# Kernel tuning notes

Hardware: AMD Instinct MI355X
Metric: run time of the kernel (lower is better)

## Reference

```python
import jax, jax.numpy as jnp
import numpy as np
from jax import lax

B, F_BINS, T = 4, 196, 1000
DM, H, DEPTH, FFN, L, EDIM = 512, 8, 64, 2048, 4, 128


def setup_inputs() -> dict:
    key = jax.random.key(0)
    ks = jax.random.split(key, 16)
    d = {}
    d['spec'] = jax.random.normal(ks[0], (B, 1, F_BINS, T), jnp.float32)
    d['conv1_w'] = jax.random.normal(ks[1], (32, 1, 5, 5), jnp.float32) / 5.0
    d['conv1_b'] = jax.random.normal(ks[2], (32,), jnp.float32) * 0.01
    d['conv2_w'] = jax.random.normal(ks[3], (64, 32, 5, 5), jnp.float32) / np.sqrt(32 * 25)
    d['conv2_b'] = jax.random.normal(ks[4], (64,), jnp.float32) * 0.01
    d['proj_w'] = jax.random.normal(ks[5], (DM, 64), jnp.float32) / 8.0
    d['proj_b'] = jnp.zeros((DM,), jnp.float32)
    d['ln1_g'] = jnp.ones((L, DM), jnp.float32)
    d['ln1_b'] = jnp.zeros((L, DM), jnp.float32)
    s = 1.0 / np.sqrt(DM)
    for i, nm in enumerate(['qw', 'kw', 'vw', 'dw']):
        d[nm] = jax.random.normal(ks[6 + i], (L, DM, DM), jnp.float32) * s
    for nm in ['qb', 'kb', 'vb', 'db']:
        d[nm] = jnp.zeros((L, DM), jnp.float32)
    d['Er'] = jax.random.normal(ks[10], (L, T, DEPTH), jnp.float32)
    d['ln2_g'] = jnp.ones((L, DM), jnp.float32)
    d['ln2_b'] = jnp.zeros((L, DM), jnp.float32)
    d['f1w'] = jax.random.normal(ks[11], (L, FFN, DM), jnp.float32) * s
    d['f1b'] = jnp.zeros((L, FFN), jnp.float32)
    d['f2w'] = jax.random.normal(ks[12], (L, DM, FFN), jnp.float32) / np.sqrt(FFN)
    d['f2b'] = jnp.zeros((L, DM), jnp.float32)
    d['deproj_w'] = jax.random.normal(ks[13], (EDIM, DM), jnp.float32) * s
    d['deproj_b'] = jnp.zeros((EDIM,), jnp.float32)
    return d


def _layernorm(x, g, b, eps=1e-5):
    mu = jnp.mean(x, -1, keepdims=True)
    var = jnp.mean(jnp.square(x - mu), -1, keepdims=True)
    return g * (x - mu) / jnp.sqrt(var + eps) + b


def _skew(QEr):
    # QEr: [B,H,S,S] -> music-transformer skew trick
    b, h, s, _ = QEr.shape
    padded = jnp.pad(QEr, ((0, 0), (0, 0), (0, 0), (1, 0)))  # [B,H,S,S+1]
    return padded.reshape(b, h, s + 1, s)[:, :, 1:, :]


def _forward(spec, conv1_w, conv1_b, conv2_w, conv2_b, proj_w, proj_b,
             ln1_g, ln1_b, qw, qb, kw, kb, vw, vb, dw, db, Er,
             ln2_g, ln2_b, f1w, f1b, f2w, f2b, deproj_w, deproj_b):
    dn = ('NCHW', 'OIHW', 'NCHW')
    x = lax.conv_general_dilated(spec, conv1_w, (1, 1), 'SAME', dimension_numbers=dn)
    x = jax.nn.gelu(x + conv1_b[None, :, None, None], approximate=False)
    x = lax.reduce_window(x, -jnp.inf, lax.max, (1, 1, 14, 1), (1, 1, 14, 1), 'VALID')
    x = lax.conv_general_dilated(x, conv2_w, (1, 1), 'SAME', dimension_numbers=dn)
    x = jax.nn.gelu(x + conv2_b[None, :, None, None], approximate=False)
    x = lax.reduce_window(x, -jnp.inf, lax.max, (1, 1, 14, 1), (1, 1, 14, 1), 'VALID')
    x = x.reshape(B, 64, T)              # freq collapsed to 1, flatten(1,2)
    x = x.transpose(0, 2, 1)             # [B,T,64]
    x = x @ proj_w.T + proj_b            # [B,T,DM]
    scale = 1.0 / np.sqrt(DEPTH)
    for l in range(L):
        xn = _layernorm(x, ln1_g[l], ln1_b[l])
        Q = (xn @ qw[l].T + qb[l]).reshape(B, T, H, DEPTH).transpose(0, 2, 1, 3)
        K = (xn @ kw[l].T + kb[l]).reshape(B, T, H, DEPTH).transpose(0, 2, 1, 3)
        V = (xn @ vw[l].T + vb[l]).reshape(B, T, H, DEPTH).transpose(0, 2, 1, 3)
        QEr = jnp.einsum('bhsd,rd->bhsr', Q, Er[l])        # relative pos scores
        Srel = _skew(QEr)
        logits = (jnp.einsum('bhsd,bhtd->bhst', Q, K) + Srel) * scale
        attn = jax.nn.softmax(logits, axis=-1)
        out = jnp.einsum('bhst,bhtd->bhsd', attn, V)
        out = out.transpose(0, 2, 1, 3).reshape(B, T, DM)
        x = x + (out @ dw[l].T + db[l])
        xn2 = _layernorm(x, ln2_g[l], ln2_b[l])
        ff = jax.nn.relu(xn2 @ f1w[l].T + f1b[l]) @ f2w[l].T + f2b[l]
        x = x + ff
    return x @ deproj_w.T + deproj_b     # [B,T,EDIM]


def reference(spec, conv1_w, conv1_b, conv2_w, conv2_b, proj_w, proj_b,
              ln1_g, ln1_b, qw, qb, kw, kb, vw, vb, dw, db, Er,
              ln2_g, ln2_b, f1w, f1b, f2w, f2b, deproj_w, deproj_b):
    return _forward(spec, conv1_w, conv1_b, conv2_w, conv2_b, proj_w, proj_b,
                    ln1_g, ln1_b, qw, qb, kw, kb, vw, vb, dw, db, Er,
                    ln2_g, ln2_b, f1w, f1b, f2w, f2b, deproj_w, deproj_b)
```

## Files before the change

### kernel.cpp

```cpp
#include <hip/hip_runtime.h>
#include <hip/hip_bf16.h>
#include <hip/hip_fp16.h>
#include <math.h>

#define BB 4
#define FBINS 196
#define TT 1000
#define DM 512
#define HH 8
#define DEPTH 64
#define FFN 2048
#define LL 4
#define EDIM 128
#define BT (BB*TT)
#define PSHIFT 12.0f

typedef __hip_bfloat16 bf16;
typedef __attribute__((ext_vector_type(8))) short short8;
typedef __attribute__((ext_vector_type(4))) float floatx4;

#define ARENA_BYTES 420000000ULL
static void* g_arena = nullptr;
__attribute__((constructor)) static void arena_init() {
    if (!g_arena) (void)hipMalloc(&g_arena, ARENA_BYTES);
}

__device__ __forceinline__ float gelu_f(float x) {
    return 0.5f * x * (1.0f + erff(x * 0.70710678118654752440f));
}

__global__ __launch_bounds__(256) void sniff_k(const unsigned short* __restrict__ p,
                                               int n, int* __restrict__ cnt) {
    int i = blockIdx.x * 256 + threadIdx.x;
    int c = 0;
    for (; i < n; i += gridDim.x * 256) {
        unsigned short u = p[i];
        if ((unsigned short)(u & 0x7FFF) > (unsigned short)0x7F80) c++;
    }
    if (c) atomicAdd(cnt, c);
}

#define NCVT 17
struct CvtArgs {
    const void* src[NCVT];
    unsigned dst[NCVT];
    unsigned cum[NCVT + 1];
    const int* cnt;
    float* dstA;
};
__global__ __launch_bounds__(256) void cvt_all(CvtArgs a) {
    unsigned i = blockIdx.x * 256 + threadIdx.x;
    if (i >= a.cum[NCVT]) return;
    bool isb = (*a.cnt == 0);
    int w = 0;
    while (i >= a.cum[w + 1]) w++;
    unsigned j = i - a.cum[w];
    float v = isb ? __bfloat162float(((const bf16*)a.src[w])[j])
                  : ((const float*)a.src[w])[j];
    a.dstA[a.dst[w] + j] = v;
}

__global__ __launch_bounds__(256) void f2bf_dyn(const void* __restrict__ src,
                                                bf16* __restrict__ d, int n,
                                                const int* __restrict__ cnt) {
    int i = blockIdx.x * 256 + threadIdx.x;
    if (i >= n) return;
    if (*cnt == 0) d[i] = ((const bf16*)src)[i];
    else           d[i] = __float2bfloat16(((const float*)src)[i]);
}

__global__ __launch_bounds__(256) void w2perm(const void* __restrict__ src,
                                              bf16* __restrict__ d,
                                              const int* __restrict__ cnt) {
    int idx = blockIdx.x * 256 + threadIdx.x;
    if (idx >= 51200) return;
    int c = idx / 800, k = idx - c * 800;
    int kc = k >> 5, ci = k & 31;
    int di = kc / 5, dj = kc - di * 5;
    int s = ((c * 32 + ci) * 5 + di) * 5 + dj;
    float v = (*cnt == 0) ? __bfloat162float(((const bf16*)src)[s])
                          : ((const float*)src)[s];
    d[idx] = __float2bfloat16(v);
}

__global__ __launch_bounds__(256) void conv1_pool2(const float* __restrict__ spec,
                                                   const float* __restrict__ w1,
                                                   const float* __restrict__ b1,
                                                   bf16* __restrict__ P1c) {
    __shared__ float ss[18][256];
    __shared__ float sw[200];
    int jt = blockIdx.x, p = blockIdx.y, z = blockIdx.z;
    int b = z >> 2, cg = z & 3;
    int tid = threadIdx.x;
    for (int i = tid; i < 200; i += 256) sw[i] = w1[cg * 200 + i];
    int ibase = p * 14, c0 = jt * 250 - 2;
    for (int idx = tid; idx < 18 * 256; idx += 256) {
        int rr = idx >> 8, cc = idx & 255;
        int gi = ibase - 2 + rr, gj = c0 + cc;
        ss[rr][cc] = (gi >= 0 && gi < FBINS && gj >= 0 && gj < TT && cc < 254)
                         ? spec[(size_t)b * FBINS * TT + (size_t)gi * TT + gj] : 0.f;
    }
    __syncthreads();
    if (tid >= 250) return;
    int j = jt * 250 + tid;
    unsigned short* orow = (unsigned short*)P1c + ((size_t)((b * 14 + p) * 1000 + j)) * 32;
    for (int cpl = 0; cpl < 8; cpl += 2) {
        int cp = cg * 8 + cpl;
        float conv[2][14];
        float b0 = b1[cp], b1v = b1[cp + 1];
#pragma unroll
        for (int i = 0; i < 14; i++) { conv[0][i] = b0; conv[1][i] = b1v; }
        const float* w0 = sw + cpl * 25;
        const float* w1p = sw + (cpl + 1) * 25;
        for (int rr = 0; rr < 18; rr++) {
            float v0 = ss[rr][tid], v1 = ss[rr][tid + 1], v2 = ss[rr][tid + 2],
                  v3 = ss[rr][tid + 3], v4 = ss[rr][tid + 4];
#pragma unroll
            for (int di = 0; di < 5; di++) {
                int i = rr - di;
                if (i >= 0 && i < 14) {
                    conv[0][i] += v0 * w0[di * 5] + v1 * w0[di * 5 + 1] + v2 * w0[di * 5 + 2]
                                + v3 * w0[di * 5 + 3] + v4 * w0[di * 5 + 4];
                    conv[1][i] += v0 * w1p[di * 5] + v1 * w1p[di * 5 + 1] + v2 * w1p[di * 5 + 2]
                                + v3 * w1p[di * 5 + 3] + v4 * w1p[di * 5 + 4];
                }
            }
        }
        float mx0 = -1e30f, mn0 = 1e30f, mx1 = -1e30f, mn1 = 1e30f;
#pragma unroll
        for (int i = 0; i < 14; i++) {
            mx0 = fmaxf(mx0, conv[0][i]); mn0 = fminf(mn0, conv[0][i]);
            mx1 = fmaxf(mx1, conv[1][i]); mn1 = fminf(mn1, conv[1][i]);
        }
        float m0 = fmaxf(gelu_f(mx0), gelu_f(mn0));
        float m1 = fmaxf(gelu_f(mx1), gelu_f(mn1));
        bf16 mb0 = __float2bfloat16(m0), mb1 = __float2bfloat16(m1);
        unsigned pk = ((unsigned)(*(unsigned short*)&mb1) << 16) |
                      (unsigned)(*(unsigned short*)&mb0);
        *(unsigned*)(orow + cp) = pk;
    }
}

__global__ __launch_bounds__(256) void conv2_gemm(const bf16* __restrict__ P1c,
                                                  const bf16* __restrict__ W2p,
                                                  const float* __restrict__ c2b,
                                                  bf16* __restrict__ convout) {
    __shared__ __align__(16) short Asm[64 * 40];
    __shared__ __align__(16) short Bsm[64 * 40];
    int tid = threadIdx.x, wave = tid >> 6, lane = tid & 63;
    int q = lane >> 4, l15 = lane & 15;
    int jt = blockIdx.x, i = blockIdx.y, b = blockIdx.z;
    int lrow = tid >> 2, lci = (tid & 3) * 8;
    int jrow = jt * 64 + lrow;
    int mw = (wave & 1) * 32, nw = (wave >> 1) * 32;
    floatx4 acc[2][2] = {};
    for (int di = 0; di < 5; di++) {
        int ii = i + di - 2;
        bool iok = (ii >= 0 && ii < 14);
        for (int dj = 0; dj < 5; dj++) {
            int kc = di * 5 + dj;
            {
                int jj = jrow + dj - 2;
                uint4 v = make_uint4(0u, 0u, 0u, 0u);
                if (iok && jrow < TT && jj >= 0 && jj < TT)
                    v = *(const uint4*)(P1c +
                        (((size_t)(b * 14 + ii)) * TT + jj) * 32 + lci);
                *(uint4*)(Asm + lrow * 40 + lci) = v;
            }
            {
                *(uint4*)(Bsm + lrow * 40 + lci) =
                    *(const uint4*)(W2p + (size_t)lrow * 800 + kc * 32 + lci);
            }
            __syncthreads();
            short8 a0 = *(const short8*)(Asm + (mw + l15) * 40 + q * 8);
            short8 a1 = *(const short8*)(Asm + (mw + 16 + l15) * 40 + q * 8);
            short8 b0 = *(const short8*)(Bsm + (nw + l15) * 40 + q * 8);
            short8 b1 = *(const short8*)(Bsm + (nw + 16 + l15) * 40 + q * 8);
            acc[0][0] = __builtin_amdgcn_mfma_f32_16x16x32_bf16(a0, b0, acc[0][0], 0, 0, 0);
            acc[0][1] = __builtin_amdgcn_mfma_f32_16x16x32_bf16(a0, b1, acc[0][1], 0, 0, 0);
            acc[1][0] = __builtin_amdgcn_mfma_f32_16x16x32_bf16(a1, b0, acc[1][0], 0, 0, 0);
            acc[1][1] = __builtin_amdgcn_mfma_f32_16x16x32_bf16(a1, b1, acc[1][1], 0, 0, 0);
            __syncthreads();
        }
    }
#pragma unroll
    for (int im = 0; im < 2; im++) {
#pragma unroll
        for (int jn = 0; jn < 2; jn++) {
            int c = nw + jn * 16 + l15;
            float bv = c2b[c];
#pragma unroll
            for (int r = 0; r < 4; r++) {
                int j = jt * 64 + mw + im * 16 + q * 4 + r;
                if (j >= TT) continue;
                convout[((size_t)(b * 14 + i) * TT + j) * 64 + c] =
                    __float2bfloat16(acc[im][jn][r] + bv);
            }
        }
    }
}

__global__ __launch_bounds__(256) void pool2_k(const bf16* __restrict__ convout,
                                               bf16* __restrict__ p2t) {
    int idx = blockIdx.x * 256 + threadIdx.x;
    if (idx >= 256000) return;
    int c = idx & 63, bj = idx >> 6;
    int b = bj / 1000, j = bj - b * 1000;
    float mx = -1e30f, mn = 1e30f;
#pragma unroll
    for (int i = 0; i < 14; i++) {
        float v = __bfloat162float(convout[((size_t)(b * 14 + i) * 1000 + j) * 64 + c]);
        mx = fmaxf(mx, v); mn = fminf(mn, v);
    }
    p2t[(size_t)bj * 64 + c] = __float2bfloat16(fmaxf(gelu_f(mx), gelu_f(mn)));
}

__global__ __launch_bounds__(256) void layernorm_k(const float* __restrict__ x,
                                                   const float* __restrict__ g,
                                                   const float* __restrict__ bta,
                                                   bf16* __restrict__ y) {
    __shared__ float red[256];
    int row = blockIdx.x, tid = threadIdx.x;
    const float* xr = x + (size_t)row * DM;
    float v0 = xr[tid], v1 = xr[tid + 256];
    red[tid] = v0 + v1;
    __syncthreads();
    for (int s = 128; s > 0; s >>= 1) { if (tid < s) red[tid] += red[tid + s]; __syncthreads(); }
    float mu = red[0] * (1.f / 512.f);
    __syncthreads();
    float d0 = v0 - mu, d1 = v1 - mu;
    red[tid] = d0 * d0 + d1 * d1;
    __syncthreads();
    for (int s = 128; s > 0; s >>= 1) { if (tid < s) red[tid] += red[tid + s]; __syncthreads(); }
    float rstd = rsqrtf(red[0] * (1.f / 512.f) + 1e-5f);
    bf16* yr = y + (size_t)row * DM;
    yr[tid]       = __float2bfloat16(d0 * rstd * g[tid]       + bta[tid]);
    yr[tid + 256] = __float2bfloat16(d1 * rstd * g[tid + 256] + bta[tid + 256]);
}

__global__ __launch_bounds__(256) void gemm_out(const float* __restrict__ A,
                                                const float* __restrict__ B,
                                                const float* __restrict__ bias,
                                                const int* __restrict__ cnt,
                                                void* __restrict__ dout,
                                                int M, int N, int K) {
    __shared__ float As[32][33];
    __shared__ float Bs[32][33];
    int tid = threadIdx.x;
    int tx = tid & 15, ty = tid >> 4;
    int m0 = blockIdx.x * 32, n0 = blockIdx.y * 32;
    float c[2][2] = {};
    for (int k0 = 0; k0 < K; k0 += 32) {
#pragma unroll
        for (int i = 0; i < 4; i++) {
            int idx = i * 256 + tid;
            int r = idx >> 5, kk = idx & 31;
            int gm = m0 + r;
            As[r][kk] = (gm < M) ? A[(size_t)gm * K + k0 + kk] : 0.f;
            Bs[r][kk] = B[(size_t)(n0 + r) * K + k0 + kk];
        }
        __syncthreads();
#pragma unroll
        for (int k = 0; k < 32; k++) {
            float a0 = As[ty * 2][k], a1 = As[ty * 2 + 1][k];
            float b0 = Bs[tx * 2][k], b1 = Bs[tx * 2 + 1][k];
            c[0][0] += a0 * b0; c[0][1] += a0 * b1;
            c[1][0] += a1 * b0; c[1][1] += a1 * b1;
        }
        __syncthreads();
    }
    bool isb = (*cnt == 0);
#pragma unroll
    for (int i = 0; i < 2; i++) {
        int m = m0 + ty * 2 + i;
        if (m >= M) continue;
#pragma unroll
        for (int jj = 0; jj < 2; jj++) {
            int n = n0 + tx * 2 + jj;
            float v = c[i][jj] + bias[n];
            if (isb) ((bf16*)dout)[(size_t)m * N + n] = __float2bfloat16(v);
            else     ((float*)dout)[(size_t)m * N + n] = v;
        }
    }
}

template <int BM, int NT, int ROUTE, int ACT, bool OUT_BF16>
__global__ __launch_bounds__(256) void mfma_big(const bf16* __restrict__ A,
                                                const bf16* __restrict__ B,
                                                const float* __restrict__ bias,
                                                const float* __restrict__ resid,
                                                float* __restrict__ Cf,
                                                bf16* __restrict__ Cb,
                                                int M, int N, int K,
                                                size_t wstride, int bstride,
                                                size_t ostride) {
    __shared__ __align__(16) short Asm[BM * 40];
    __shared__ __align__(16) short Bsm[NT * 40];
    int tid = threadIdx.x, wave = tid >> 6, lane = tid & 63;
    int q = lane >> 4, l15 = lane & 15;
    int m0 = blockIdx.x * BM, n0 = blockIdx.y * NT;
    int lrow = tid >> 2, lk = (tid & 3) * 8;
    constexpr int MF = (NT == 128) ? (BM / 16) : (BM / 32);
    int m0w = (NT == 128) ? 0 : ((wave >> 1) * (BM / 2));
    int nfb = (NT == 128) ? (wave * 32) : ((wave & 1) * 32);
    floatx4 acc[MF][2] = {};
    for (int k0 = 0; k0 < K; k0 += 32) {
#pragma unroll
        for (int hh = 0; hh < BM / 64; hh++) {
            int row = lrow + hh * 64, gm = m0 + row;
            uint4 v = make_uint4(0u, 0u, 0u, 0u);
            if (gm < M) v = *(const uint4*)(A + (size_t)gm * K + k0 + lk);
            *(uint4*)(Asm + row * 40 + lk) = v;
        }
#pragma unroll
        for (int hh = 0; hh < NT / 64; hh++) {
            int row = lrow + hh * 64, gn = n0 + row;
            const bf16* src = ROUTE
                ? B + (size_t)(gn >> 9) * wstride + (size_t)(gn & 511) * K + k0 + lk
                : B + (size_t)gn * K + k0 + lk;
            *(uint4*)(Bsm + row * 40 + lk) = *(const uint4*)src;
        }
        __syncthreads();
        short8 a[MF], b2[2];
#pragma unroll
        for (int im = 0; im < MF; im++)
            a[im] = *(const short8*)(Asm + (m0w + im * 16 + l15) * 40 + q * 8);
#pragma unroll
        for (int jn = 0; jn < 2; jn++)
            b2[jn] = *(const short8*)(Bsm + (nfb + jn * 16 + l15) * 40 + q * 8);
#pragma unroll
        for (int im = 0; im < MF; im++)
#pragma unroll
            for (int jn = 0; jn < 2; jn++)
                acc[im][jn] = __builtin_amdgcn_mfma_f32_16x16x32_bf16(
                    a[im], b2[jn], acc[im][jn], 0, 0, 0);
        __syncthreads();
    }
#pragma unroll
    for (int im = 0; im < MF; im++) {
#pragma unroll
        for (int jn = 0; jn < 2; jn++) {
            int nn = n0 + nfb + jn * 16 + l15;
            float bval = ROUTE ? bias[(nn >> 9) * bstride + (nn & 511)] : bias[nn];
#pragma unroll
            for (int r = 0; r < 4; r++) {
                int m = m0 + m0w + im * 16 + q * 4 + r;
                if (m >= M) continue;
                float v = acc[im][jn][r] + bval;
                if (resid) v += resid[(size_t)m * N + nn];
                if (ACT == 1) v = fmaxf(v, 0.f);
                if (ROUTE)
                    Cb[(size_t)(nn >> 9) * ostride + (size_t)m * 512 + (nn & 511)] =
                        __float2bfloat16(v);
                else if (OUT_BF16)
                    Cb[(size_t)m * N + nn] = __float2bfloat16(v);
                else
                    Cf[(size_t)m * N + nn] = v;
            }
        }
    }
}

__global__ __launch_bounds__(256) void vt_k(const bf16* __restrict__ Vb,
                                            bf16* __restrict__ Vt) {
    __shared__ short tile[64][65];
    int t0 = blockIdx.x * 64, z = blockIdx.y;
    int b = z >> 3, h = z & 7;
    int tid = threadIdx.x;
#pragma unroll
    for (int i = 0; i < 16; i++) {
        int tr = i * 4 + (tid >> 6), d = tid & 63;
        int t = t0 + tr;
        bf16 v = (t < TT) ? Vb[((size_t)b * TT + t) * DM + h * 64 + d] : (bf16)__float2bfloat16(0.f);
        tile[tr][d] = *(short*)&v;
    }
    __syncthreads();
#pragma unroll
    for (int i = 0; i < 16; i++) {
        int dr = i * 4 + (tid >> 6), tc = tid & 63;
        *(short*)&Vt[(size_t)z * 65536 + dr * 1024 + t0 + tc] = tile[tc][dr];
    }
}

__global__ __launch_bounds__(256, 2) void attn_fused(const bf16* __restrict__ Q,
                                                     const bf16* __restrict__ K,
                                                     const bf16* __restrict__ Er,
                                                     const bf16* __restrict__ Vt,
                                                     bf16* __restrict__ AO) {
    __shared__ __align__(16) short Qs[6400];
    __shared__ __align__(16) short pool[12800];
    __shared__ __align__(16) short Pl[64 * 136];
    __shared__ __align__(16) short Vs[64 * 136];
    __shared__ float rsw[4][64];
    int tid = threadIdx.x, wave = tid >> 6, lane = tid & 63;
    int q = lane >> 4, l15 = lane & 15;
    int m0 = blockIdx.x * 64;
    int z = blockIdx.z, b = z >> 3, h = z & 7;
    const bf16* Ap = Q + (size_t)b * TT * DM + h * 64;
    const bf16* Bp = K + (size_t)b * TT * DM + h * 64;
    const bf16* Vp = Vt + (size_t)z * 65536;
    int lrow = tid >> 2, lk = (tid & 3) * 8;
    int mw = wave * 16;

#pragma unroll
    for (int kh = 0; kh < 2; kh++) {
        int gm = m0 + lrow;
        uint4 v = make_uint4(0u, 0u, 0u, 0u);
        if (gm < TT) v = *(const uint4*)(Ap + (size_t)gm * DM + kh * 32 + lk);
        *(uint4*)(Qs + kh * 3200 + lrow * 40 + lk) = v;
        if (tid < 64) {
            int rr = 64 + (tid >> 2);
            int g2 = m0 + rr;
            uint4 v2 = make_uint4(0u, 0u, 0u, 0u);
            if (g2 < TT) v2 = *(const uint4*)(Ap + (size_t)g2 * DM + kh * 32 + lk);
            *(uint4*)(Qs + kh * 3200 + rr * 40 + lk) = v2;
        }
    }

    float rsum[4] = {0.f, 0.f, 0.f, 0.f};
    floatx4 accO[4] = {};

    for (int tc = 0; tc < 8; tc++) {
        int t0 = tc * 128;
        int db = t0 - m0 - 64;
        floatx4 accS[2][4] = {};
        floatx4 accG[5][3] = {};
        for (int k0 = 0; k0 < 64; k0 += 32) {
            {
                int gn = t0 + lrow;
                uint4 v0 = make_uint4(0u, 0u, 0u, 0u), v1 = v0;
                if (gn < TT)      v0 = *(const uint4*)(Bp + (size_t)gn * DM + k0 + lk);
                if (gn + 64 < TT) v1 = *(const uint4*)(Bp + (size_t)(gn + 64) * DM + k0 + lk);
                *(uint4*)(pool + lrow * 40 + lk) = v0;
                *(uint4*)(pool + (lrow + 64) * 40 + lk) = v1;
            }
            {
#pragma unroll
                for (int hh = 0; hh < 3; hh++) {
                    int dd = lrow + hh * 64;
                    int dl = db + dd;
                    int src = (dl <= 0) ? (999 + dl) : (dl - 1);
                    uint4 v = make_uint4(0u, 0u, 0u, 0u);
                    if (src >= 0 && src < TT)
                        v = *(const uint4*)(Er + (size_t)src * 64 + k0 + lk);
                    *(uint4*)(pool + 5120 + dd * 40 + lk) = v;
                }
            }
            if (k0 == 0) {
#pragma unroll
                for (int e = 0; e < 4; e++) {
                    int li = tid + e * 256;
                    int row = li >> 4, cs = (li & 15) * 8;
                    *(uint4*)(Vs + row * 136 + cs) =
                        *(const uint4*)(Vp + (size_t)row * 1024 + t0 + cs);
                }
            }
            __syncthreads();
            short8 qf[5], kf[2], e[3];
#pragma unroll
            for (int im = 0; im < 5; im++)
                qf[im] = *(const short8*)(Qs + (k0 >> 5) * 3200 + (im * 16 + l15) * 40 + q * 8);
#pragma unroll
            for (int i = 0; i < 2; i++)
                kf[i] = *(const short8*)(pool + ((2 * wave + i) * 16 + l15) * 40 + q * 8);
#pragma unroll
            for (int jg = 0; jg < 3; jg++)
                e[jg] = *(const short8*)(pool + 5120 + (wave * 48 + jg * 16 + l15) * 40 + q * 8);
#pragma unroll
            for (int i = 0; i < 2; i++)
#pragma unroll
                for (int j = 0; j < 4; j++)
                    accS[i][j] = __builtin_amdgcn_mfma_f32_16x16x32_bf16(
                        kf[i], qf[j], accS[i][j], 0, 0, 0);
#pragma unroll
            for (int im = 0; im < 5; im++)
#pragma unroll
                for (int jg = 0; jg < 3; jg++)
                    accG[im][jg] = __builtin_amdgcn_mfma_f32_16x16x32_bf16(
                        qf[im], e[jg], accG[im][jg], 0, 0, 0);
            __syncthreads();
        }
#pragma unroll
        for (int jg = 0; jg < 3; jg++) {
            int dd = wave * 48 + jg * 16 + l15;
            int delta = dd + db;
            int nlb = dd - 64;
#pragma unroll
            for (int im = 0; im < 5; im++) {
#pragma unroll
                for (int r = 0; r < 4; r++) {
                    int ur = im * 16 + q * 4 + r;
                    int nl = ur + nlb;
                    if (nl >= 0 && nl < 128) {
                        int mr = (delta <= 0) ? ur : (ur - 1);
                        if (mr >= 0 && mr < 64) {
                            bf16 gb = __float2bfloat16(accG[im][jg][r]);
                            Pl[mr * 136 + nl] = *(short*)&gb;
                        }
                        if (delta == 0 && ur >= 1 && ur <= 64)
                            Pl[(ur - 1) * 136 + nl] = 0;
                    }
                }
            }
        }
        __syncthreads();
#pragma unroll
        for (int i = 0; i < 2; i++) {
            int nt = (2 * wave + i) * 16 + q * 4;
#pragma unroll
            for (int j = 0; j < 4; j++) {
                int ml = j * 16 + l15;
                uint2 rq = *(const uint2*)(Pl + ml * 136 + nt);
                unsigned short rh[4] = {
                    (unsigned short)(rq.x & 0xFFFF), (unsigned short)(rq.x >> 16),
                    (unsigned short)(rq.y & 0xFFFF), (unsigned short)(rq.y >> 16)};
                unsigned short o4[4];
#pragma unroll
                for (int r = 0; r < 4; r++) {
                    int n = t0 + nt + r;
                    float rel = __bfloat162float(*(bf16*)&rh[r]);
                    float pv = __expf((accS[i][j][r] + rel) * 0.125f - PSHIFT);
                    pv = (n < TT) ? pv : 0.f;
                    rsum[j] += pv;
                    bf16 pb = __float2bfloat16(pv);
                    o4[r] = *(unsigned short*)&pb;
                }
                uint2 w;
                w.x = (unsigned)o4[0] | ((unsigned)o4[1] << 16);
                w.y = (unsigned)o4[2] | ((unsigned)o4[3] << 16);
                *(uint2*)(Pl + ml * 136 + nt) = w;
            }
        }
        __syncthreads();
#pragma unroll
        for (int kc = 0; kc < 4; kc++) {
            short8 a = *(const short8*)(Pl + (mw + l15) * 136 + kc * 32 + q * 8);
#pragma unroll
            for (int jn = 0; jn < 4; jn++) {
                short8 bv = *(const short8*)(Vs + (jn * 16 + l15) * 136 + kc * 32 + q * 8);
                accO[jn] = __builtin_amdgcn_mfma_f32_16x16x32_bf16(a, bv, accO[jn], 0, 0, 0);
            }
        }
        __syncthreads();
    }
#pragma unroll
    for (int j = 0; j < 4; j++) {
        float s = rsum[j];
        s += __shfl_xor(s, 16, 64);
        s += __shfl_xor(s, 32, 64);
        if (q == 0) rsw[wave][j * 16 + l15] = s;
    }
    __syncthreads();
#pragma unroll
    for (int r = 0; r < 4; r++) {
        int lm = mw + q * 4 + r;
        int m = m0 + lm;
        if (m >= TT) continue;
        float inv = 1.f / (rsw[0][lm] + rsw[1][lm] + rsw[2][lm] + rsw[3][lm]);
#pragma unroll
        for (int jn = 0; jn < 4; jn++)
            AO[((size_t)b * TT + m) * DM + h * 64 + jn * 16 + l15] =
                __float2bfloat16(accO[jn][r] * inv);
    }
}

extern "C" void kernel_launch(void* const* d_in, const int* in_sizes, int n_in,
                              void* d_out, int out_size, void* d_ws, size_t ws_size,
                              hipStream_t stream) {
    if (!g_arena) (void)hipMalloc(&g_arena, ARENA_BYTES);
    float* A = (float*)g_arena;

    static const unsigned off[27] = {
        0, 784000, 784800, 784832, 836032, 836096, 868864, 869376, 871424,
        873472, 1922048, 2970624, 4019200, 5067776, 5069824, 5071872,
        5073920, 5075968, 5331968, 5334016, 5336064, 9530368, 9538560,
        13732864, 13734912, 13800448, 13800576};
    const float* spec  = A + off[0];
    const float* c1w   = A + off[1];
    const float* c1b   = A + off[2];
    const float* c2b   = A + off[4];
    const float* projb = A + off[6];
    const float* ln1g  = A + off[7];
    const float* ln1b  = A + off[8];
    const float* qb    = A + off[13];
    const float* db    = A + off[16];
    const float* ln2g  = A + off[18];
    const float* ln2b  = A + off[19];
    const float* f1b   = A + off[21];
    const float* f2b_  = A + off[23];
    const float* depw  = A + off[24];
    const float* depb  = A + off[25];

    const size_t PA = 13800576;
    float* x    = A + PA;
    float* P1   = x + 2048000;
    float* SM   = P1 + 1792000;
    bf16* P1c     = (bf16*)P1;
    bf16* p2t_b   = (bf16*)SM;
    bf16* projw_b = (bf16*)(SM + 128000);
    bf16* w2p     = (bf16*)(SM + 150000);
    int*   cnt  = (int*)(SM + 256000);
    float* ScF  = SM + 256004;
    float* B0   = ScF + 32000000;
    bf16* wb_qkvd = (bf16*)B0;
    bf16* wb_f1   = (bf16*)(B0 + 2097152);
    bf16* wb_f2   = (bf16*)(B0 + 4194304);
    bf16* Erb     = (bf16*)(B0 + 6291456);
    bf16* xn_b    = (bf16*)(B0 + 6419456);
    bf16* AO_b    = (bf16*)(B0 + 7443456);
    bf16* Qb_b    = (bf16*)(B0 + 8467456);
    bf16* Kb_b    = (bf16*)(B0 + 9491456);
    bf16* Vb_b    = (bf16*)(B0 + 10515456);
    bf16* FFH_b   = (bf16*)(B0 + 11539456);
    bf16* Vt      = (bf16*)(B0 + 15635456);
    bf16* convout = (bf16*)(B0 + 16684032);

    hipMemsetAsync(cnt, 0, sizeof(int), stream);
    sniff_k<<<1024, 256, 0, stream>>>((const unsigned short*)d_in[20], 1000000, cnt);

    static const int cvt_ids[NCVT] = {0, 1, 2, 4, 6, 7, 8, 13, 14, 15, 16,
                                      18, 19, 21, 23, 24, 25};
    CvtArgs ca;
    unsigned cum = 0;
    for (int t = 0; t < NCVT; t++) {
        int w = cvt_ids[t];
        ca.src[t] = d_in[w];
        ca.dst[t] = off[w];
        ca.cum[t] = cum;
        cum += off[w + 1] - off[w];
    }
    ca.cum[NCVT] = cum;
    ca.cnt = cnt; ca.dstA = A;
    cvt_all<<<(cum + 255) / 256, 256, 0, stream>>>(ca);

    for (int t = 0; t < 4; t++)
        f2bf_dyn<<<4096, 256, 0, stream>>>(d_in[9 + t], wb_qkvd + (size_t)t * 1048576,
                                           1048576, cnt);
    f2bf_dyn<<<16384, 256, 0, stream>>>(d_in[20], wb_f1, 4194304, cnt);
    f2bf_dyn<<<16384, 256, 0, stream>>>(d_in[22], wb_f2, 4194304, cnt);
    f2bf_dyn<<<1000,  256, 0, stream>>>(d_in[17], Erb,   256000, cnt);
    f2bf_dyn<<<128,   256, 0, stream>>>(d_in[5],  projw_b, 32768, cnt);
    w2perm<<<200, 256, 0, stream>>>(d_in[3], w2p, cnt);

    conv1_pool2<<<dim3(4, 14, 16), 256, 0, stream>>>(spec, c1w, c1b, P1c);
    conv2_gemm<<<dim3(16, 14, 4), 256, 0, stream>>>(P1c, w2p, c2b, convout);
    pool2_k<<<1000, 256, 0, stream>>>(convout, p2t_b);
    mfma_big<64, 64, 0, 0, false><<<dim3(63, 8), 256, 0, stream>>>(
        p2t_b, projw_b, projb, nullptr, x, nullptr, BT, DM, 64, 0, 0, 0);

    for (int l = 0; l < LL; l++) {
        layernorm_k<<<BT, 256, 0, stream>>>(x, ln1g + l * DM, ln1b + l * DM, xn_b);
        mfma_big<128, 128, 1, 0, true><<<dim3(32, 12), 256, 0, stream>>>(
            xn_b, wb_qkvd + (size_t)l * DM * DM, qb + l * DM, nullptr,
            nullptr, Qb_b, BT, 1536, DM, 1048576, 2048, 2048000);
        vt_k<<<dim3(16, 32), 256, 0, stream>>>(Vb_b, Vt);
        attn_fused<<<dim3(16, 1, 32), 256, 0, stream>>>(
            Qb_b, Kb_b, Erb + (size_t)l * TT * DEPTH, Vt, AO_b);
        mfma_big<64, 64, 0, 0, false><<<dim3(63, 8), 256, 0, stream>>>(
            AO_b, wb_qkvd + 3 * 1048576 + (size_t)l * DM * DM, db + l * DM, x,
            x, nullptr, BT, DM, DM, 0, 0, 0);
        layernorm_k<<<BT, 256, 0, stream>>>(x, ln2g + l * DM, ln2b + l * DM, xn_b);
        mfma_big<128, 128, 0, 1, true><<<dim3(32, 16), 256, 0, stream>>>(
            xn_b, wb_f1 + (size_t)l * FFN * DM, f1b + l * FFN, nullptr,
            nullptr, FFH_b, BT, FFN, DM, 0, 0, 0);
        mfma_big<64, 64, 0, 0, false><<<dim3(63, 8), 256, 0, stream>>>(
            FFH_b, wb_f2 + (size_t)l * DM * FFN, f2b_ + l * DM, x,
            x, nullptr, BT, DM, FFN, 0, 0, 0);
    }

    gemm_out<<<dim3(125, 4), 256, 0, stream>>>(x, depw, depb, cnt, d_out, BT, EDIM, DM);
}
```

Baseline: 1.211 ms.

## Split attention tile into separate relative-position and QK phases to cut register pressure

The fused per-tile loop that computed both the Q·Er relative-position GEMM and the Q·K GEMM over two k-halves is split into sequential phases. First the full Er slice is staged and the relative scores are computed and scattered into the skewed Pl buffer. Then K and V are loaded and QK scores are computed. Only one set of accumulators is live at a time, which lowers VGPR pressure, and the shared pool grows to hold full 64-deep rows with a 72-element stride. The cost is an extra barrier per tile and less overlap between the two GEMMs.

Result: faster. 1.105 ms (-8.8%).

```diff
diff --git a/kernel.cpp b/kernel.cpp
--- a/kernel.cpp
+++ b/kernel.cpp
@@ -388,7 +388,7 @@
                                                      const bf16* __restrict__ Vt,
                                                      bf16* __restrict__ AO) {
     __shared__ __align__(16) short Qs[6400];
-    __shared__ __align__(16) short pool[12800];
+    __shared__ __align__(16) short pool[13824];
     __shared__ __align__(16) short Pl[64 * 136];
     __shared__ __align__(16) short Vs[64 * 136];
     __shared__ float rsw[4][64];
@@ -423,87 +423,105 @@
     for (int tc = 0; tc < 8; tc++) {
         int t0 = tc * 128;
         int db = t0 - m0 - 64;
+
+        {
+#pragma unroll
+            for (int hh = 0; hh < 3; hh++) {
+                int dd = lrow + hh * 64;
+                int dl = db + dd;
+                int src = (dl <= 0) ? (999 + dl) : (dl - 1);
+                bool ok = (src >= 0 && src < TT);
+#pragma unroll
+                for (int kh = 0; kh < 2; kh++) {
+                    uint4 v = make_uint4(0u, 0u, 0u, 0u);
+                    if (ok) v = *(const uint4*)(Er + (size_t)src * 64 + kh * 32 + lk);
+                    *(uint4*)(pool + dd * 72 + kh * 32 + lk) = v;
+                }
+            }
+            __syncthreads();
+            floatx4 accG[5][3] = {};
+#pragma unroll
+            for (int kh = 0; kh < 2; kh++) {
+                short8 qf[5], e[3];
+#pragma unroll
+                for (int im = 0; im < 5; im++)
+                    qf[im] = *(const short8*)(Qs + kh * 3200 + (im * 16 + l15) * 40 + q * 8);
+#pragma unroll
+                for (int jg = 0; jg < 3; jg++)
+                    e[jg] = *(const short8*)(pool + (wave * 48 + jg * 16 + l15) * 72 + kh * 32 + q * 8);
+#pragma unroll
+                for (int im = 0; im < 5; im++)
+#pragma unroll
+                    for (int jg = 0; jg < 3; jg++)
+                        accG[im][jg] = __builtin_amdgcn_mfma_f32_16x16x32_bf16(
+                            qf[im], e[jg], accG[im][jg], 0, 0, 0);
+            }
+#pragma unroll
+            for (int jg = 0; jg < 3; jg++) {
+                int dd = wave * 48 + jg * 16 + l15;
+                int delta = dd + db;
+                int nlb = dd - 64;
+#pragma unroll
+                for (int im = 0; im < 5; im++) {
+#pragma unroll
+                    for (int r = 0; r < 4; r++) {
+                        int ur = im * 16 + q * 4 + r;
+                        int nl = ur + nlb;
+                        if (nl >= 0 && nl < 128) {
+                            int mr = (delta <= 0) ? ur : (ur - 1);
+                            if (mr >= 0 && mr < 64) {
+                                bf16 gb = __float2bfloat16(accG[im][jg][r]);
+                                Pl[mr * 136 + nl] = *(short*)&gb;
+                            }
+                            if (delta == 0 && ur >= 1 && ur <= 64)
+                                Pl[(ur - 1) * 136 + nl] = 0;
+                        }
+                    }
+                }
+            }
+        }
+        __syncthreads();
+
+        {
+#pragma unroll
+            for (int hh = 0; hh < 2; hh++) {
+                int row = lrow + hh * 64;
+                int gn = t0 + row;
+                bool ok = (gn < TT);
+#pragma unroll
+                for (int kh = 0; kh < 2; kh++) {
+                    uint4 v = make_uint4(0u, 0u, 0u, 0u);
+                    if (ok) v = *(const uint4*)(Bp + (size_t)gn * DM + kh * 32 + lk);
+                    *(uint4*)(pool + row * 72 + kh * 32 + lk) = v;
+                }
+            }
+#pragma unroll
+            for (int e2 = 0; e2 < 4; e2++) {
+                int li = tid + e2 * 256;
+                int row = li >> 4, cs = (li & 15) * 8;
+                *(uint4*)(Vs + row * 136 + cs) =
+                    *(const uint4*)(Vp + (size_t)row * 1024 + t0 + cs);
+            }
+        }
+        __syncthreads();
+
         floatx4 accS[2][4] = {};
-        floatx4 accG[5][3] = {};
-        for (int k0 = 0; k0 < 64; k0 += 32) {
-            {
-                int gn = t0 + lrow;
-                uint4 v0 = make_uint4(0u, 0u, 0u, 0u), v1 = v0;
-                if (gn < TT)      v0 = *(const uint4*)(Bp + (size_t)gn * DM + k0 + lk);
-                if (gn + 64 < TT) v1 = *(const uint4*)(Bp + (size_t)(gn + 64) * DM + k0 + lk);
-                *(uint4*)(pool + lrow * 40 + lk) = v0;
-                *(uint4*)(pool + (lrow + 64) * 40 + lk) = v1;
-            }
-            {
-#pragma unroll
-                for (int hh = 0; hh < 3; hh++) {
-                    int dd = lrow + hh * 64;
-                    int dl = db + dd;
-                    int src = (dl <= 0) ? (999 + dl) : (dl - 1);
-                    uint4 v = make_uint4(0u, 0u, 0u, 0u);
-                    if (src >= 0 && src < TT)
-                        v = *(const uint4*)(Er + (size_t)src * 64 + k0 + lk);
-                    *(uint4*)(pool + 5120 + dd * 40 + lk) = v;
-                }
-            }
-            if (k0 == 0) {
-#pragma unroll
-                for (int e = 0; e < 4; e++) {
-                    int li = tid + e * 256;
-                    int row = li >> 4, cs = (li & 15) * 8;
-                    *(uint4*)(Vs + row * 136 + cs) =
-                        *(const uint4*)(Vp + (size_t)row * 1024 + t0 + cs);
-                }
-            }
-            __syncthreads();
-            short8 qf[5], kf[2], e[3];
-#pragma unroll
-            for (int im = 0; im < 5; im++)
-                qf[im] = *(const short8*)(Qs + (k0 >> 5) * 3200 + (im * 16 + l15) * 40 + q * 8);
+#pragma unroll
+        for (int kh = 0; kh < 2; kh++) {
+            short8 qf[4], kf[2];
+#pragma unroll
+            for (int j = 0; j < 4; j++)
+                qf[j] = *(const short8*)(Qs + kh * 3200 + (j * 16 + l15) * 40 + q * 8);
 #pragma unroll
             for (int i = 0; i < 2; i++)
-                kf[i] = *(const short8*)(pool + ((2 * wave + i) * 16 + l15) * 40 + q * 8);
-#pragma unroll
-            for (int jg = 0; jg < 3; jg++)
-                e[jg] = *(const short8*)(pool + 5120 + (wave * 48 + jg * 16 + l15) * 40 + q * 8);
+                kf[i] = *(const short8*)(pool + ((2 * wave + i) * 16 + l15) * 72 + kh * 32 + q * 8);
 #pragma unroll
             for (int i = 0; i < 2; i++)
 #pragma unroll
                 for (int j = 0; j < 4; j++)
                     accS[i][j] = __builtin_amdgcn_mfma_f32_16x16x32_bf16(
                         kf[i], qf[j], accS[i][j], 0, 0, 0);
-#pragma unroll
-            for (int im = 0; im < 5; im++)
-#pragma unroll
-                for (int jg = 0; jg < 3; jg++)
-                    accG[im][jg] = __builtin_amdgcn_mfma_f32_16x16x32_bf16(
-                        qf[im], e[jg], accG[im][jg], 0, 0, 0);
-            __syncthreads();
-        }
-#pragma unroll
-        for (int jg = 0; jg < 3; jg++) {
-            int dd = wave * 48 + jg * 16 + l15;
-            int delta = dd + db;
-            int nlb = dd - 64;
-#pragma unroll
-            for (int im = 0; im < 5; im++) {
-#pragma unroll
-                for (int r = 0; r < 4; r++) {
-                    int ur = im * 16 + q * 4 + r;
-                    int nl = ur + nlb;
-                    if (nl >= 0 && nl < 128) {
-                        int mr = (delta <= 0) ? ur : (ur - 1);
-                        if (mr >= 0 && mr < 64) {
-                            bf16 gb = __float2bfloat16(accG[im][jg][r]);
-                            Pl[mr * 136 + nl] = *(short*)&gb;
-                        }
-                        if (delta == 0 && ur >= 1 && ur <= 64)
-                            Pl[(ur - 1) * 136 + nl] = 0;
-                    }
-                }
-            }
-        }
-        __syncthreads();
+        }
 #pragma unroll
         for (int i = 0; i < 2; i++) {
             int nt = (2 * wave + i) * 16 + q * 4;
```
